# Optimization experiments

Measured on AMD Instinct MI355X. Metric: run time of the kernel, lower is better.

The kernel has to match this reference:

```python
import jax, jax.numpy as jnp
import numpy as np

B, S, D, F, E, NS, K = 2, 1024, 1024, 4096, 8, 8, 2
FS = F // NS  # shared-expert hidden size = d_ff // num_shared_experts


def setup_inputs() -> dict:
    key = jax.random.key(0)
    ks = jax.random.split(key, 8)
    scale = 0.02
    return {
        "hidden_states": jax.random.normal(ks[0], (B, S, D), jnp.float32),
        "gate_W": jax.random.normal(ks[1], (E, D), jnp.float32) * scale,
        "w1_e": jax.random.normal(ks[2], (E, D, F), jnp.float32) * scale,
        "w3_e": jax.random.normal(ks[3], (E, D, F), jnp.float32) * scale,
        "w2_e": jax.random.normal(ks[4], (E, F, D), jnp.float32) * scale,
        "w1_s": jax.random.normal(ks[5], (NS, D, FS), jnp.float32) * scale,
        "w3_s": jax.random.normal(ks[6], (NS, D, FS), jnp.float32) * scale,
        "w2_s": jax.random.normal(ks[7], (NS, FS, D), jnp.float32) * scale,
    }


def reference(hidden_states, gate_W, w1_e, w3_e, w2_e, w1_s, w3_s, w2_s):
    b, s, d = hidden_states.shape
    e = gate_W.shape[0]
    flat = hidden_states.reshape(-1, d)            # [T, D]
    T = flat.shape[0]

    # --- gate: softmax over experts, top-k probs scattered (k=0 slot only survives) ---
    logits = (flat @ gate_W.T).astype(jnp.float32)  # [T, E]
    probs = jax.nn.softmax(logits, axis=-1)
    top_v, top_i = jax.lax.top_k(probs, K)          # [T, K]
    gates = jnp.zeros((T, e), probs.dtype).at[jnp.arange(T)[:, None], top_i].set(top_v)

    # --- routed experts: module runs every expert densely on all tokens ---
    g = jax.nn.silu(jnp.einsum('td,edf->etf', flat, w1_e))  # [E, T, F]
    u = jnp.einsum('td,edf->etf', flat, w3_e)
    out_e = jnp.einsum('etf,efd->etd', g * u, w2_e)         # [E, T, D]
    routed = jnp.einsum('te,etd->td', gates, out_e).reshape(b, s, d)

    # --- shared experts (mean over NS experts) ---
    gs = jax.nn.silu(jnp.einsum('bsd,ndf->nbsf', hidden_states, w1_s))
    us = jnp.einsum('bsd,ndf->nbsf', hidden_states, w3_s)
    shared = jnp.einsum('nbsf,nfd->bsd', gs * us, w2_s) / w1_s.shape[0]

    alpha = 0.5
    return alpha * shared + (1.0 - alpha) * routed
```

## Files before the change

kernel.cpp:

```cpp
#include <hip/hip_runtime.h>

#define T 2048
#define D 1024
#define F 4096
#define E 8
#define NS 8
#define FS 512
#define SHB 5120
#define NROWS 7168
#define MT_MAX 56

typedef float floatx4 __attribute__((ext_vector_type(4)));
typedef short short8 __attribute__((ext_vector_type(8)));

__device__ __forceinline__ unsigned short f2bf(float f) {
  unsigned int u = __float_as_uint(f);
  u += 0x7FFF + ((u >> 16) & 1);
  return (unsigned short)(u >> 16);
}

__device__ __forceinline__ void glds16(const void* g, void* l) {
  __builtin_amdgcn_global_load_lds(
      (const __attribute__((address_space(1))) void*)g,
      (__attribute__((address_space(3))) void*)l, 16, 0, 0);
}

__global__ void gate_kernel(const float* __restrict__ x, const float* __restrict__ gW,
                            unsigned short* __restrict__ xb, int* __restrict__ cnt,
                            int* __restrict__ list_tok, float* __restrict__ list_gate) {
  int t = blockIdx.x, tid = threadIdx.x;
  const float* xr = x + (size_t)t * D;
  float acc[E];
#pragma unroll
  for (int e = 0; e < E; ++e) acc[e] = 0.f;
  for (int d = tid; d < D; d += 256) {
    float xv = xr[d];
    xb[(size_t)t * D + d] = f2bf(xv);
#pragma unroll
    for (int e = 0; e < E; ++e) acc[e] += xv * gW[e * D + d];
  }
#pragma unroll
  for (int o = 32; o > 0; o >>= 1)
#pragma unroll
    for (int e = 0; e < E; ++e) acc[e] += __shfl_down(acc[e], o, 64);
  __shared__ float wred[4][E];
  int lane = tid & 63, wv = tid >> 6;
  if (lane == 0)
#pragma unroll
    for (int e = 0; e < E; ++e) wred[wv][e] = acc[e];
  __syncthreads();
  if (tid == 0) {
    float l[E];
#pragma unroll
    for (int e = 0; e < E; ++e) l[e] = wred[0][e] + wred[1][e] + wred[2][e] + wred[3][e];
    int i1 = 0; float m1 = l[0];
    for (int e = 1; e < E; ++e) if (l[e] > m1) { m1 = l[e]; i1 = e; }
    int i2 = -1; float m2 = -3.4e38f;
    for (int e = 0; e < E; ++e) if (e != i1 && l[e] > m2) { m2 = l[e]; i2 = e; }
    float s = 0.f, p[E];
#pragma unroll
    for (int e = 0; e < E; ++e) { p[e] = __expf(l[e] - m1); s += p[e]; }
    float inv = 1.f / s;
    int p1 = atomicAdd(&cnt[i1], 1);
    list_tok[i1 * T + p1] = t; list_gate[i1 * T + p1] = p[i1] * inv;
    int p2 = atomicAdd(&cnt[i2], 1);
    list_tok[i2 * T + p2] = t; list_gate[i2 * T + p2] = p[i2] * inv;
  }
}

__global__ void offsets_kernel(const int* __restrict__ cnt, int* __restrict__ off,
                               int* __restrict__ mt_expert) {
  if (threadIdx.x == 0 && blockIdx.x == 0) {
    int o = 0;
    for (int e = 0; e < E; ++e) { off[e] = o; o += (cnt[e] + 127) & ~127; }
    off[E] = o;
    for (int i = 0; i < MT_MAX; ++i) mt_expert[i] = -1;
    for (int e = 0; e < E; ++e) {
      int t0 = off[e] >> 7, nt = (cnt[e] + 127) >> 7;
      for (int i = 0; i < nt; ++i) mt_expert[t0 + i] = e;
    }
    for (int i = SHB >> 7; i < MT_MAX; ++i) mt_expert[i] = E;
  }
}

__global__ void scatter_kernel(const int* __restrict__ cnt, const int* __restrict__ off,
                               const int* __restrict__ list_tok, const float* __restrict__ list_gate,
                               int* __restrict__ tok_of_row, float* __restrict__ row_scale,
                               int* __restrict__ tok_rows, int* __restrict__ tk) {
  int idx = blockIdx.x * 256 + threadIdx.x;
  int e = idx >> 11, i = idx & (T - 1);
  if (e < E && i < cnt[e]) {
    int row = off[e] + i;
    int t = list_tok[e * T + i];
    tok_of_row[row] = t;
    row_scale[row] = 0.5f * list_gate[e * T + i];
    int k = atomicAdd(&tk[t], 1);
    tok_rows[2 * t + k] = row;
  }
}

__global__ void transpose_cast(const float* __restrict__ in, unsigned short* __restrict__ out,
                               int R, int C) {
  in += (size_t)blockIdx.z * R * C;
  out += (size_t)blockIdx.z * R * C;
  int r0 = blockIdx.y * 32, c0 = blockIdx.x * 32;
  __shared__ float tile[32][33];
  int tid = threadIdx.x;
  {
    int rl = tid >> 3, cl = (tid & 7) * 4;
    float4 v = *(const float4*)(in + (size_t)(r0 + rl) * C + c0 + cl);
    tile[rl][cl] = v.x; tile[rl][cl + 1] = v.y;
    tile[rl][cl + 2] = v.z; tile[rl][cl + 3] = v.w;
  }
  __syncthreads();
  {
    int cl = tid >> 3, rq = (tid & 7) * 4;
    int c = c0 + cl, r = r0 + rq;
    ushort4 v;
    v.x = f2bf(tile[rq][cl]);     v.y = f2bf(tile[rq + 1][cl]);
    v.z = f2bf(tile[rq + 2][cl]); v.w = f2bf(tile[rq + 3][cl]);
    int Rt = R >> 5;
    size_t o = ((size_t)(c >> 7) * Rt + (r >> 5)) * 4096 + (size_t)(c & 127) * 32 + (r & 31);
    *(ushort4*)(out + o) = v;
  }
}

__global__ __launch_bounds__(256, 2) void up_gemm(
    const unsigned short* __restrict__ xb, const unsigned short* __restrict__ W1T,
    const unsigned short* __restrict__ W3T, const unsigned short* __restrict__ W1sT,
    const unsigned short* __restrict__ W3sT, const int* __restrict__ mt_expert,
    const int* __restrict__ tok_of_row, unsigned short* __restrict__ Hb) {
  int mt = blockIdx.y, ntile = blockIdx.x;
  int e = mt_expert[mt];
  if (e < 0) return;
  const unsigned short *B1, *B3;
  if (e < E) {
    B1 = W1T + (size_t)e * F * D;
    B3 = W3T + (size_t)e * F * D;
  } else {
    B1 = W1sT; B3 = W3sT;
  }
  __shared__ unsigned short Al[128 * 32];
  __shared__ unsigned short B1l[128 * 32];
  __shared__ unsigned short B3l[128 * 32];
  int tid = threadIdx.x;
  int lane = tid & 63, wv = tid >> 6, wm = wv >> 1, wn = wv & 1;
  int row16 = lane & 15, quad = lane >> 4;
  int qsw8 = ((lane >> 4) ^ ((lane >> 1) & 3)) * 8;
  int swzb = (tid & ~3) * 16 + (((tid & 3) ^ ((tid >> 3) & 3)) * 16);

  int ar = tid >> 1;
  int hrow_s = mt * 128 + ar;
  int srow = (e < E) ? tok_of_row[hrow_s] : (hrow_s - SHB);
  int ja = (tid & 1) * 2;
  int sa = (tid >> 2) & 3;
  const uint4* aptr = (const uint4*)(xb + (size_t)srow * D) + ja;
  uint4* alds0 = (uint4*)Al + ar * 4 + (ja ^ sa);
  uint4* alds1 = (uint4*)Al + ar * 4 + ((ja + 1) ^ sa);

  const unsigned short* b1t = B1 + (size_t)ntile * (D / 32) * 4096;
  const unsigned short* b3t = B3 + (size_t)ntile * (D / 32) * 4096;

  floatx4 accg[4][4], accu[4][4];
#pragma unroll
  for (int i = 0; i < 4; ++i)
#pragma unroll
    for (int j = 0; j < 4; ++j) {
      accg[i][j] = (floatx4){0.f, 0.f, 0.f, 0.f};
      accu[i][j] = (floatx4){0.f, 0.f, 0.f, 0.f};
    }
  int lw = wv * 1024;
  for (int kt = 0; kt < D / 32; ++kt) {
    uint4 av0 = aptr[0];
    uint4 av1 = aptr[1];
    const char* b1s = (const char*)(b1t + (size_t)kt * 4096);
    const char* b3s = (const char*)(b3t + (size_t)kt * 4096);
    glds16(b1s + swzb, (char*)B1l + lw);
    glds16(b1s + 4096 + swzb, (char*)B1l + 4096 + lw);
    glds16(b3s + swzb, (char*)B3l + lw);
    glds16(b3s + 4096 + swzb, (char*)B3l + 4096 + lw);
    alds0[0] = av0; alds1[0] = av1;
    __syncthreads();
    short8 af[4], b1f[4], b3f[4];
#pragma unroll
    for (int mi = 0; mi < 4; ++mi)
      af[mi] = *(const short8*)(Al + (wm * 64 + mi * 16 + row16) * 32 + qsw8);
#pragma unroll
    for (int ni = 0; ni < 4; ++ni) {
      b1f[ni] = *(const short8*)(B1l + (wn * 64 + ni * 16 + row16) * 32 + qsw8);
      b3f[ni] = *(const short8*)(B3l + (wn * 64 + ni * 16 + row16) * 32 + qsw8);
    }
#pragma unroll
    for (int mi = 0; mi < 4; ++mi)
#pragma unroll
      for (int ni = 0; ni < 4; ++ni) {
        accg[mi][ni] = __builtin_amdgcn_mfma_f32_16x16x32_bf16(af[mi], b1f[ni], accg[mi][ni], 0, 0, 0);
        accu[mi][ni] = __builtin_amdgcn_mfma_f32_16x16x32_bf16(af[mi], b3f[ni], accu[mi][ni], 0, 0, 0);
      }
    aptr += 4;
    __syncthreads();
  }
#pragma unroll
  for (int mi = 0; mi < 4; ++mi)
#pragma unroll
    for (int ni = 0; ni < 4; ++ni)
#pragma unroll
      for (int r = 0; r < 4; ++r) {
        int hrow = mt * 128 + wm * 64 + mi * 16 + quad * 4 + r;
        int col = ntile * 128 + wn * 64 + ni * 16 + row16;
        float g = accg[mi][ni][r], u = accu[mi][ni][r];
        float h = g * u / (1.0f + __expf(-g));
        size_t o = ((size_t)(hrow >> 7) * 128 + (col >> 5)) * 4096 + (size_t)(hrow & 127) * 32 + (col & 31);
        Hb[o] = f2bf(h);
      }
}

__global__ __launch_bounds__(256, 2) void down_gemm(
    const unsigned short* __restrict__ Hb, const unsigned short* __restrict__ W2T,
    const unsigned short* __restrict__ W2sT, const int* __restrict__ mt_expert,
    const float* __restrict__ row_scale, float* __restrict__ O) {
  int mt = blockIdx.y, ntile = blockIdx.x, kz = blockIdx.z;
  int e = mt_expert[mt];
  if (e < 0) return;
  const unsigned short* Bt = ((e < E) ? (W2T + (size_t)e * D * F) : W2sT)
                             + (size_t)ntile * (F / 32) * 4096;
  const unsigned short* At = Hb + (size_t)mt * (F / 32) * 4096;
  O += (size_t)kz * NROWS * D;
  __shared__ unsigned short Al[128 * 32];
  __shared__ unsigned short Bl[128 * 32];
  int tid = threadIdx.x;
  int lane = tid & 63, wv = tid >> 6, wm = wv >> 1, wn = wv & 1;
  int row16 = lane & 15, quad = lane >> 4;
  int qsw8 = ((lane >> 4) ^ ((lane >> 1) & 3)) * 8;
  int swzb = (tid & ~3) * 16 + (((tid & 3) ^ ((tid >> 3) & 3)) * 16);
  floatx4 acc[4][4];
#pragma unroll
  for (int i = 0; i < 4; ++i)
#pragma unroll
    for (int j = 0; j < 4; ++j) acc[i][j] = (floatx4){0.f, 0.f, 0.f, 0.f};
  int lw = wv * 1024;
  for (int kt = kz * 64; kt < kz * 64 + 64; ++kt) {
    const char* as = (const char*)(At + (size_t)kt * 4096);
    const char* bs = (const char*)(Bt + (size_t)kt * 4096);
    glds16(as + swzb, (char*)Al + lw);
    glds16(as + 4096 + swzb, (char*)Al + 4096 + lw);
    glds16(bs + swzb, (char*)Bl + lw);
    glds16(bs + 4096 + swzb, (char*)Bl + 4096 + lw);
    __syncthreads();
    short8 af[4], bf[4];
#pragma unroll
    for (int mi = 0; mi < 4; ++mi)
      af[mi] = *(const short8*)(Al + (wm * 64 + mi * 16 + row16) * 32 + qsw8);
#pragma unroll
    for (int ni = 0; ni < 4; ++ni)
      bf[ni] = *(const short8*)(Bl + (wn * 64 + ni * 16 + row16) * 32 + qsw8);
#pragma unroll
    for (int mi = 0; mi < 4; ++mi)
#pragma unroll
      for (int ni = 0; ni < 4; ++ni)
        acc[mi][ni] = __builtin_amdgcn_mfma_f32_16x16x32_bf16(af[mi], bf[ni], acc[mi][ni], 0, 0, 0);
    __syncthreads();
  }
#pragma unroll
  for (int mi = 0; mi < 4; ++mi)
#pragma unroll
    for (int ni = 0; ni < 4; ++ni)
#pragma unroll
      for (int r = 0; r < 4; ++r) {
        int grow = mt * 128 + wm * 64 + mi * 16 + quad * 4 + r;
        int col = ntile * 128 + wn * 64 + ni * 16 + row16;
        float scale = (grow < SHB) ? row_scale[grow] : 0.0625f;
        O[(size_t)grow * D + col] = acc[mi][ni][r] * scale;
      }
}

__global__ void combine_kernel(const float* __restrict__ O, const int* __restrict__ tok_rows,
                               float* __restrict__ out) {
  int idx = blockIdx.x * 256 + threadIdx.x;
  int t = idx >> 8, c = idx & 255;
  int r0 = tok_rows[2 * t], r1 = tok_rows[2 * t + 1];
  const float4* O4 = (const float4*)O;
  const size_t HLF = (size_t)NROWS * 256;
  float4 a = O4[(size_t)r0 * 256 + c];
  float4 b = O4[(size_t)r1 * 256 + c];
  float4 s = O4[((size_t)SHB + t) * 256 + c];
  float4 a2 = O4[HLF + (size_t)r0 * 256 + c];
  float4 b2 = O4[HLF + (size_t)r1 * 256 + c];
  float4 s2 = O4[HLF + ((size_t)SHB + t) * 256 + c];
  float4 r;
  r.x = a.x + b.x + s.x + a2.x + b2.x + s2.x;
  r.y = a.y + b.y + s.y + a2.y + b2.y + s2.y;
  r.z = a.z + b.z + s.z + a2.z + b2.z + s2.z;
  r.w = a.w + b.w + s.w + a2.w + b2.w + s2.w;
  ((float4*)out)[idx] = r;
}

extern "C" void kernel_launch(void* const* d_in, const int* in_sizes, int n_in,
                              void* d_out, int out_size, void* d_ws, size_t ws_size,
                              hipStream_t stream) {
  (void)in_sizes; (void)n_in; (void)out_size; (void)ws_size;
  const float* x   = (const float*)d_in[0];
  const float* gW  = (const float*)d_in[1];
  const float* w1e = (const float*)d_in[2];
  const float* w3e = (const float*)d_in[3];
  const float* w2e = (const float*)d_in[4];
  const float* w1s = (const float*)d_in[5];
  const float* w3s = (const float*)d_in[6];
  const float* w2s = (const float*)d_in[7];
  float* out = (float*)d_out;

  char* w = (char*)d_ws;
  auto alloc = [&](size_t bytes) {
    char* p = w; w += (bytes + 255) & ~(size_t)255; return p;
  };
  unsigned short* xb   = (unsigned short*)alloc((size_t)T * D * 2);
  unsigned short* W1T  = (unsigned short*)alloc((size_t)E * F * D * 2);
  unsigned short* W3T  = (unsigned short*)alloc((size_t)E * F * D * 2);
  unsigned short* W2T  = (unsigned short*)alloc((size_t)E * D * F * 2);
  unsigned short* W1sT = (unsigned short*)alloc((size_t)F * D * 2);
  unsigned short* W3sT = (unsigned short*)alloc((size_t)F * D * 2);
  unsigned short* W2sT = (unsigned short*)alloc((size_t)D * F * 2);
  unsigned short* Hb   = (unsigned short*)alloc((size_t)NROWS * F * 2);
  float* Ob        = (float*)alloc((size_t)2 * NROWS * D * 4);
  float* row_scale = (float*)alloc((size_t)SHB * 4);
  float* list_gate = (float*)alloc((size_t)E * T * 4);
  int* list_tok    = (int*)alloc((size_t)E * T * 4);
  int* tok_rows    = (int*)alloc((size_t)T * 2 * 4);
  int* offv        = (int*)alloc(16 * 4);
  int* mt_expert   = (int*)alloc(64 * 4);
  int* ctrl        = (int*)alloc((size_t)(8 + T + SHB) * 4);
  int* cnt = ctrl; int* tk = ctrl + 8; int* tok_of_row = ctrl + 8 + T;

  hipMemsetAsync(ctrl, 0, (size_t)(8 + T + SHB) * 4, stream);
  gate_kernel<<<T, 256, 0, stream>>>(x, gW, xb, cnt, list_tok, list_gate);
  offsets_kernel<<<1, 64, 0, stream>>>(cnt, offv, mt_expert);
  scatter_kernel<<<(E * T) / 256, 256, 0, stream>>>(cnt, offv, list_tok, list_gate,
                                                    tok_of_row, row_scale, tok_rows, tk);
  transpose_cast<<<dim3(F / 32, D / 32, E), 256, 0, stream>>>(w1e, W1T, D, F);
  transpose_cast<<<dim3(F / 32, D / 32, E), 256, 0, stream>>>(w3e, W3T, D, F);
  transpose_cast<<<dim3(D / 32, F / 32, E), 256, 0, stream>>>(w2e, W2T, F, D);
  transpose_cast<<<dim3(FS / 32, D / 32, NS), 256, 0, stream>>>(w1s, W1sT, D, FS);
  transpose_cast<<<dim3(FS / 32, D / 32, NS), 256, 0, stream>>>(w3s, W3sT, D, FS);
  transpose_cast<<<dim3(D / 32, F / 32, 1), 256, 0, stream>>>(w2s, W2sT, F, D);
  up_gemm<<<dim3(F / 128, MT_MAX), 256, 0, stream>>>(xb, W1T, W3T, W1sT, W3sT,
                                                     mt_expert, tok_of_row, Hb);
  down_gemm<<<dim3(D / 128, MT_MAX, 2), 256, 0, stream>>>(Hb, W2T, W2sT, mt_expert, row_scale, Ob);
  combine_kernel<<<(T * D / 4) / 256, 256, 0, stream>>>(Ob, tok_rows, out);
}
```

Baseline: 742.6 us.

## Double-buffer LDS tiles in up and down GEMMs and load A directly to LDS

```diff
diff --git a/kernel.cpp b/kernel.cpp
--- a/kernel.cpp
+++ b/kernel.cpp
@@ -140,26 +140,25 @@
   } else {
     B1 = W1sT; B3 = W3sT;
   }
-  __shared__ unsigned short Al[128 * 32];
-  __shared__ unsigned short B1l[128 * 32];
-  __shared__ unsigned short B3l[128 * 32];
+  __shared__ unsigned short Al[2][128 * 32];
+  __shared__ unsigned short B1l[2][128 * 32];
+  __shared__ unsigned short B3l[2][128 * 32];
   int tid = threadIdx.x;
   int lane = tid & 63, wv = tid >> 6, wm = wv >> 1, wn = wv & 1;
   int row16 = lane & 15, quad = lane >> 4;
-  int qsw8 = ((lane >> 4) ^ ((lane >> 1) & 3)) * 8;
-  int swzb = (tid & ~3) * 16 + (((tid & 3) ^ ((tid >> 3) & 3)) * 16);
-
-  int ar = tid >> 1;
-  int hrow_s = mt * 128 + ar;
-  int srow = (e < E) ? tok_of_row[hrow_s] : (hrow_s - SHB);
-  int ja = (tid & 1) * 2;
-  int sa = (tid >> 2) & 3;
-  const uint4* aptr = (const uint4*)(xb + (size_t)srow * D) + ja;
-  uint4* alds0 = (uint4*)Al + ar * 4 + (ja ^ sa);
-  uint4* alds1 = (uint4*)Al + ar * 4 + ((ja + 1) ^ sa);
-
-  const unsigned short* b1t = B1 + (size_t)ntile * (D / 32) * 4096;
-  const unsigned short* b3t = B3 + (size_t)ntile * (D / 32) * 4096;
+  int qsw8 = (quad ^ ((lane >> 1) & 3)) * 8;
+  int swzb = (tid >> 2) * 64 + (((tid & 3) ^ ((tid >> 3) & 3)) * 16);
+  int lw = wv * 1024;
+
+  int r1 = tid >> 2;
+  int hrow1 = mt * 128 + r1, hrow2 = hrow1 + 64;
+  int srow1 = (e < E) ? tok_of_row[hrow1] : (hrow1 - SHB);
+  int srow2 = (e < E) ? tok_of_row[hrow2] : (hrow2 - SHB);
+  int asl = ((tid & 3) ^ ((tid >> 3) & 3)) * 16;
+  const char* asrc1 = (const char*)(xb + (size_t)srow1 * D) + asl;
+  const char* asrc2 = (const char*)(xb + (size_t)srow2 * D) + asl;
+  const char* b1t = (const char*)(B1 + (size_t)ntile * (D / 32) * 4096);
+  const char* b3t = (const char*)(B3 + (size_t)ntile * (D / 32) * 4096);
 
   floatx4 accg[4][4], accu[4][4];
 #pragma unroll
@@ -169,26 +168,34 @@
       accg[i][j] = (floatx4){0.f, 0.f, 0.f, 0.f};
       accu[i][j] = (floatx4){0.f, 0.f, 0.f, 0.f};
     }
-  int lw = wv * 1024;
+
+  auto stage = [&](int kt, int b) {
+    size_t ko = (size_t)kt * 64;
+    size_t bo = (size_t)kt * 8192;
+    glds16(asrc1 + ko, (char*)Al[b] + lw);
+    glds16(asrc2 + ko, (char*)Al[b] + 4096 + lw);
+    glds16(b1t + bo + swzb, (char*)B1l[b] + lw);
+    glds16(b1t + bo + 4096 + swzb, (char*)B1l[b] + 4096 + lw);
+    glds16(b3t + bo + swzb, (char*)B3l[b] + lw);
+    glds16(b3t + bo + 4096 + swzb, (char*)B3l[b] + 4096 + lw);
+  };
+
+  stage(0, 0);
+  __syncthreads();
+  int cur = 0;
   for (int kt = 0; kt < D / 32; ++kt) {
-    uint4 av0 = aptr[0];
-    uint4 av1 = aptr[1];
-    const char* b1s = (const char*)(b1t + (size_t)kt * 4096);
-    const char* b3s = (const char*)(b3t + (size_t)kt * 4096);
-    glds16(b1s + swzb, (char*)B1l + lw);
-    glds16(b1s + 4096 + swzb, (char*)B1l + 4096 + lw);
-    glds16(b3s + swzb, (char*)B3l + lw);
-    glds16(b3s + 4096 + swzb, (char*)B3l + 4096 + lw);
-    alds0[0] = av0; alds1[0] = av1;
-    __syncthreads();
+    if (kt + 1 < D / 32) stage(kt + 1, cur ^ 1);
+    const unsigned short* Ac = Al[cur];
+    const unsigned short* B1c = B1l[cur];
+    const unsigned short* B3c = B3l[cur];
     short8 af[4], b1f[4], b3f[4];
 #pragma unroll
     for (int mi = 0; mi < 4; ++mi)
-      af[mi] = *(const short8*)(Al + (wm * 64 + mi * 16 + row16) * 32 + qsw8);
+      af[mi] = *(const short8*)(Ac + (wm * 64 + mi * 16 + row16) * 32 + qsw8);
 #pragma unroll
     for (int ni = 0; ni < 4; ++ni) {
-      b1f[ni] = *(const short8*)(B1l + (wn * 64 + ni * 16 + row16) * 32 + qsw8);
-      b3f[ni] = *(const short8*)(B3l + (wn * 64 + ni * 16 + row16) * 32 + qsw8);
+      b1f[ni] = *(const short8*)(B1c + (wn * 64 + ni * 16 + row16) * 32 + qsw8);
+      b3f[ni] = *(const short8*)(B3c + (wn * 64 + ni * 16 + row16) * 32 + qsw8);
     }
 #pragma unroll
     for (int mi = 0; mi < 4; ++mi)
@@ -197,8 +204,8 @@
         accg[mi][ni] = __builtin_amdgcn_mfma_f32_16x16x32_bf16(af[mi], b1f[ni], accg[mi][ni], 0, 0, 0);
         accu[mi][ni] = __builtin_amdgcn_mfma_f32_16x16x32_bf16(af[mi], b3f[ni], accu[mi][ni], 0, 0, 0);
       }
-    aptr += 4;
     __syncthreads();
+    cur ^= 1;
   }
 #pragma unroll
   for (int mi = 0; mi < 4; ++mi)
@@ -222,44 +229,54 @@
   int mt = blockIdx.y, ntile = blockIdx.x, kz = blockIdx.z;
   int e = mt_expert[mt];
   if (e < 0) return;
-  const unsigned short* Bt = ((e < E) ? (W2T + (size_t)e * D * F) : W2sT)
-                             + (size_t)ntile * (F / 32) * 4096;
-  const unsigned short* At = Hb + (size_t)mt * (F / 32) * 4096;
+  const char* Bt = (const char*)(((e < E) ? (W2T + (size_t)e * D * F) : W2sT)
+                                 + (size_t)ntile * (F / 32) * 4096);
+  const char* At = (const char*)(Hb + (size_t)mt * (F / 32) * 4096);
   O += (size_t)kz * NROWS * D;
-  __shared__ unsigned short Al[128 * 32];
-  __shared__ unsigned short Bl[128 * 32];
+  __shared__ unsigned short Al[2][128 * 32];
+  __shared__ unsigned short Bl[2][128 * 32];
   int tid = threadIdx.x;
   int lane = tid & 63, wv = tid >> 6, wm = wv >> 1, wn = wv & 1;
   int row16 = lane & 15, quad = lane >> 4;
-  int qsw8 = ((lane >> 4) ^ ((lane >> 1) & 3)) * 8;
-  int swzb = (tid & ~3) * 16 + (((tid & 3) ^ ((tid >> 3) & 3)) * 16);
+  int qsw8 = (quad ^ ((lane >> 1) & 3)) * 8;
+  int swzb = (tid >> 2) * 64 + (((tid & 3) ^ ((tid >> 3) & 3)) * 16);
+  int lw = wv * 1024;
   floatx4 acc[4][4];
 #pragma unroll
   for (int i = 0; i < 4; ++i)
 #pragma unroll
     for (int j = 0; j < 4; ++j) acc[i][j] = (floatx4){0.f, 0.f, 0.f, 0.f};
-  int lw = wv * 1024;
-  for (int kt = kz * 64; kt < kz * 64 + 64; ++kt) {
-    const char* as = (const char*)(At + (size_t)kt * 4096);
-    const char* bs = (const char*)(Bt + (size_t)kt * 4096);
-    glds16(as + swzb, (char*)Al + lw);
-    glds16(as + 4096 + swzb, (char*)Al + 4096 + lw);
-    glds16(bs + swzb, (char*)Bl + lw);
-    glds16(bs + 4096 + swzb, (char*)Bl + 4096 + lw);
-    __syncthreads();
+
+  auto stage = [&](int kt, int b) {
+    size_t o = (size_t)kt * 8192;
+    glds16(At + o + swzb, (char*)Al[b] + lw);
+    glds16(At + o + 4096 + swzb, (char*)Al[b] + 4096 + lw);
+    glds16(Bt + o + swzb, (char*)Bl[b] + lw);
+    glds16(Bt + o + 4096 + swzb, (char*)Bl[b] + 4096 + lw);
+  };
+
+  int k0 = kz * 64, kend = k0 + 64;
+  stage(k0, 0);
+  __syncthreads();
+  int cur = 0;
+  for (int kt = k0; kt < kend; ++kt) {
+    if (kt + 1 < kend) stage(kt + 1, cur ^ 1);
+    const unsigned short* Ac = Al[cur];
+    const unsigned short* Bc = Bl[cur];
     short8 af[4], bf[4];
 #pragma unroll
     for (int mi = 0; mi < 4; ++mi)
-      af[mi] = *(const short8*)(Al + (wm * 64 + mi * 16 + row16) * 32 + qsw8);
+      af[mi] = *(const short8*)(Ac + (wm * 64 + mi * 16 + row16) * 32 + qsw8);
 #pragma unroll
     for (int ni = 0; ni < 4; ++ni)
-      bf[ni] = *(const short8*)(Bl + (wn * 64 + ni * 16 + row16) * 32 + qsw8);
+      bf[ni] = *(const short8*)(Bc + (wn * 64 + ni * 16 + row16) * 32 + qsw8);
 #pragma unroll
     for (int mi = 0; mi < 4; ++mi)
 #pragma unroll
       for (int ni = 0; ni < 4; ++ni)
         acc[mi][ni] = __builtin_amdgcn_mfma_f32_16x16x32_bf16(af[mi], bf[ni], acc[mi][ni], 0, 0, 0);
     __syncthreads();
+    cur ^= 1;
   }
 #pragma unroll
   for (int mi = 0; mi < 4; ++mi)
```

Measured after the change: 768.5 us. +3.5%, slower.
